# Optimization experiments

Measured on AMD Instinct MI355X. Metric: run time of the kernel, lower is better.

Reference implementation:

```python
import jax, jax.numpy as jnp
import numpy as np


def _hilbert_envelope(x1d):
    """|analytic signal| of a real 1-D signal, matching scipy.signal.hilbert."""
    N = x1d.shape[0]  # static at trace time
    h = np.zeros(N, dtype=np.float32)
    if N % 2 == 0:
        h[0] = 1.0
        h[N // 2] = 1.0
        h[1:N // 2] = 2.0
    else:
        h[0] = 1.0
        h[1:(N + 1) // 2] = 2.0
    Xf = jnp.fft.fft(x1d)
    analytic = jnp.fft.ifft(Xf * jnp.asarray(h))
    return jnp.abs(analytic)


def setup_inputs() -> dict:
    key = jax.random.key(0)
    B, L, D = 32, 4096, 64
    x = jax.random.normal(key, (B, L, D), dtype=jnp.float32)
    return {"x": x}


def reference(x):
    B, L, D = x.shape
    flat = x.reshape(-1)  # [B*L*D], one long signal as in the original
    up = jnp.clip(flat, 0.0, None)
    down = jnp.clip(-flat, 0.0, None)
    envelope_max = _hilbert_envelope(up).reshape(B, L, D)
    envelope_min = (-_hilbert_envelope(down)).reshape(B, L, D)
    avg_envelope = (envelope_max + envelope_min) * 0.5
    imf = x - avg_envelope
    # torch.std(dim=1, unbiased=True) -> ddof=1 over the time axis
    std_res = jnp.std(imf, axis=1, keepdims=True, ddof=1) + jnp.float32(0.01)
    return imf / std_res, avg_envelope
```

## Files before the change

kernel.cpp:

```cpp
#include <hip/hip_runtime.h>
#include <math.h>

#define NTOT 8388608
#define N1   2048
#define N2   4096
#define BB   32
#define LL   4096
#define DD   64

enum { M_NONE = 0, M_TW = 1, M_SCALE = 4 };

__device__ inline float2 cmul(float2 a, float2 b) {
    return make_float2(a.x*b.x - a.y*b.y, a.x*b.y + a.y*b.x);
}
__device__ inline float2 cmul_conj(float2 a, float2 b) {
    return make_float2(a.x*b.x + a.y*b.y, a.y*b.x - a.x*b.y);
}
__device__ inline float2 cadd(float2 a, float2 b){ return make_float2(a.x+b.x, a.y+b.y); }
__device__ inline float2 csub(float2 a, float2 b){ return make_float2(a.x-b.x, a.y-b.y); }
__device__ inline float2 mul_pi(float2 a){ return make_float2(-a.y, a.x); }
__device__ inline float2 mul_mi(float2 a){ return make_float2(a.y, -a.x); }
__device__ inline int pidx(int a){ return a + (a >> 4); }

template<bool INV>
__device__ inline void dft8(const float2* x, float2* y) {
    const float C = 0.70710678118654752f;
    float2 t0=cadd(x[0],x[4]), t1=cadd(x[1],x[5]), t2=cadd(x[2],x[6]), t3=cadd(x[3],x[7]);
    float2 u0=csub(x[0],x[4]), u1=csub(x[1],x[5]), u2=csub(x[2],x[6]), u3=csub(x[3],x[7]);
    if (!INV) {
        u1 = make_float2(C*(u1.x+u1.y), C*(u1.y-u1.x));
        u2 = mul_mi(u2);
        u3 = make_float2(C*(u3.y-u3.x), -C*(u3.x+u3.y));
    } else {
        u1 = make_float2(C*(u1.x-u1.y), C*(u1.y+u1.x));
        u2 = mul_pi(u2);
        u3 = make_float2(-C*(u3.x+u3.y), C*(u3.x-u3.y));
    }
    {
        float2 s0=cadd(t0,t2), s1=cadd(t1,t3), d0=csub(t0,t2);
        float2 d1 = INV ? mul_pi(csub(t1,t3)) : mul_mi(csub(t1,t3));
        y[0]=cadd(s0,s1); y[4]=csub(s0,s1); y[2]=cadd(d0,d1); y[6]=csub(d0,d1);
    }
    {
        float2 s0=cadd(u0,u2), s1=cadd(u1,u3), d0=csub(u0,u2);
        float2 d1 = INV ? mul_pi(csub(u1,u3)) : mul_mi(csub(u1,u3));
        y[1]=cadd(s0,s1); y[5]=csub(s0,s1); y[3]=cadd(d0,d1); y[7]=csub(d0,d1);
    }
}

__device__ inline void dft8_h0_inv(const float2* x, float2* y) {
    const float C = 0.70710678118654752f;
    float2 u1 = make_float2(C*(x[1].x - x[1].y), C*(x[1].y + x[1].x));
    float2 u2 = mul_pi(x[2]);
    float2 u3 = make_float2(-C*(x[3].x + x[3].y), C*(x[3].x - x[3].y));
    {
        float2 s0=cadd(x[0],x[2]), s1=cadd(x[1],x[3]), d0=csub(x[0],x[2]);
        float2 d1 = mul_pi(csub(x[1],x[3]));
        y[0]=cadd(s0,s1); y[4]=csub(s0,s1); y[2]=cadd(d0,d1); y[6]=csub(d0,d1);
    }
    {
        float2 s0=cadd(x[0],u2), s1=cadd(u1,u3), d0=csub(x[0],u2);
        float2 d1 = mul_pi(csub(u1,u3));
        y[1]=cadd(s0,s1); y[5]=csub(s0,s1); y[3]=cadd(d0,d1); y[7]=csub(d0,d1);
    }
}

template<bool INV>
__device__ inline void dft4(const float2* u, float2* y) {
    float2 s0=cadd(u[0],u[2]), s1=cadd(u[1],u[3]), d0=csub(u[0],u[2]);
    float2 d1 = INV ? mul_pi(csub(u[1],u[3])) : mul_mi(csub(u[1],u[3]));
    y[0]=cadd(s0,s1); y[2]=csub(s0,s1); y[1]=cadd(d0,d1); y[3]=csub(d0,d1);
}

template<bool INV, int SH>
__device__ inline void twiddle8(float2* y, int ps, const float2* __restrict__ T1t) {
    float2 w1 = T1t[(ps << SH) & 4095];
    float2 w2 = cmul(w1, w1);
    float2 w3 = cmul(w2, w1);
    float2 w4 = cmul(w2, w2);
    float2 w5 = cmul(w4, w1);
    float2 w6 = cmul(w3, w3);
    float2 w7 = cmul(w4, w3);
    if (!INV) {
        y[1]=cmul(y[1],w1); y[2]=cmul(y[2],w2); y[3]=cmul(y[3],w3);
        y[4]=cmul(y[4],w4); y[5]=cmul(y[5],w5); y[6]=cmul(y[6],w6); y[7]=cmul(y[7],w7);
    } else {
        y[1]=cmul_conj(y[1],w1); y[2]=cmul_conj(y[2],w2); y[3]=cmul_conj(y[3],w3);
        y[4]=cmul_conj(y[4],w4); y[5]=cmul_conj(y[5],w5); y[6]=cmul_conj(y[6],w6); y[7]=cmul_conj(y[7],w7);
    }
}

__global__ __launch_bounds__(256) void gen_tables(float2* T1, float2* T2) {
    int j = blockIdx.x * 256 + threadIdx.x;
    if (j < 4096) {
        double ang = -2.0 * M_PI * (double)j / 4096.0;
        T1[j] = make_float2((float)cos(ang), (float)sin(ang));
    } else if (j < 4096 + 2048) {
        int b = j - 4096;
        double ang = -2.0 * M_PI * (double)b / 8388608.0;
        T2[b] = make_float2((float)cos(ang), (float)sin(ang));
    }
}

__device__ inline float2 wbig(int t, const float2* __restrict__ T1t, const float2* __restrict__ T2t) {
    return cmul(T1t[t >> 11], T2t[t & 2047]);
}

template<bool INV, int MODE>
__global__ __launch_bounds__(512) void fft4096(float2* data,
                                               const float2* __restrict__ T1t,
                                               const float2* __restrict__ T2t) {
    __shared__ float2 S[4352];
    const int t = threadIdx.x;
    const int r = blockIdx.x;
    float2* base = data + (size_t)r * 4096;

    float2 x[8], y[8];
    #pragma unroll
    for (int m = 0; m < 8; ++m) x[m] = base[t + 512*m];

    #pragma unroll
    for (int st = 0; st < 3; ++st) {
        const int s = 1 << (3*st);
        const int q = t & (s - 1);
        const int ps = t - q;
        dft8<INV>(x, y);
        twiddle8<INV, 0>(y, ps, T1t);
        if (st) __syncthreads();
        #pragma unroll
        for (int k = 0; k < 8; ++k) S[pidx(8*ps + q + k*s)] = y[k];
        __syncthreads();
        #pragma unroll
        for (int m = 0; m < 8; ++m) x[m] = S[pidx(t + 512*m)];
    }
    dft8<INV>(x, y);

    if (MODE == M_TW) {
        float2 wb    = wbig(r * t, T1t, T2t);
        float2 wstep = wbig(512 * r, T1t, T2t);
        #pragma unroll
        for (int k = 0; k < 8; ++k) {
            int o = t + 512*k;
            base[o] = INV ? cmul_conj(y[k], wb) : cmul(y[k], wb);
            wb = INV ? cmul_conj(wb, wstep) : cmul(wb, wstep);
        }
    } else {
        #pragma unroll
        for (int k = 0; k < 8; ++k) {
            int o = t + 512*k;
            float2 v = y[k];
            if (MODE == M_SCALE) {
                const float sc = 1.f / 8388608.f;
                v.x *= sc; v.y *= sc;
            }
            base[o] = v;
        }
    }
}

__global__ __launch_bounds__(256) void fftmid(float2* data,
                                              const float2* __restrict__ T1t,
                                              const float2* __restrict__ T2t) {
    __shared__ float2 S[2176];
    const int t = threadIdx.x;
    const int r = blockIdx.x;
    float2* base = data + (size_t)r * 2048;

    float2 x[8], y[8];
    #pragma unroll
    for (int m = 0; m < 8; ++m) x[m] = base[t + 256*m];

    #pragma unroll
    for (int st = 0; st < 3; ++st) {
        const int s = 1 << (3*st);
        const int q = t & (s - 1);
        const int ps = t - q;
        dft8<false>(x, y);
        twiddle8<false, 1>(y, ps, T1t);
        if (st) __syncthreads();
        #pragma unroll
        for (int k = 0; k < 8; ++k) S[pidx(8*ps + q + k*s)] = y[k];
        __syncthreads();
        if (st < 2) {
            #pragma unroll
            for (int m = 0; m < 8; ++m) x[m] = S[pidx(t + 256*m)];
        }
    }
    float2 xa[4], xb[4], ya[4], yb[4];
    #pragma unroll
    for (int m = 0; m < 4; ++m) {
        xa[m] = S[pidx(t + 512*m)];
        xb[m] = S[pidx(t + 256 + 512*m)];
    }
    dft4<false>(xa, ya);
    dft4<false>(xb, yb);
    __syncthreads();
    #pragma unroll
    for (int k = 0; k < 4; ++k) {
        int o = t + 512*k;
        if (o < 1024) {
            float h = (o == 0 && r == 0) ? 1.f : 2.f;
            S[pidx(o)] = make_float2(ya[k].x * h, ya[k].y * h);
        } else if (o == 1024) {
            S[pidx(1024)] = (r == 0) ? ya[k] : make_float2(0.f, 0.f);
        }
        int o2 = o + 256;
        if (o2 < 1024) S[pidx(o2)] = make_float2(yb[k].x * 2.f, yb[k].y * 2.f);
    }
    __syncthreads();
    #pragma unroll
    for (int m = 0; m < 4; ++m) x[m] = S[pidx(t + 256*m)];
    dft8_h0_inv(x, y);
    if (t == 0) {
        float2 c = S[pidx(1024)];
        #pragma unroll
        for (int k = 0; k < 8; ++k) {
            if (k & 1) { y[k].x -= c.x; y[k].y -= c.y; }
            else       { y[k].x += c.x; y[k].y += c.y; }
        }
    }
    twiddle8<true, 1>(y, t, T1t);
    __syncthreads();
    #pragma unroll
    for (int k = 0; k < 8; ++k) S[pidx(8*t + k)] = y[k];
    __syncthreads();
    #pragma unroll
    for (int st = 1; st < 3; ++st) {
        const int s = 1 << (3*st);
        const int q = t & (s - 1);
        const int ps = t - q;
        #pragma unroll
        for (int m = 0; m < 8; ++m) x[m] = S[pidx(t + 256*m)];
        dft8<true>(x, y);
        twiddle8<true, 1>(y, ps, T1t);
        __syncthreads();
        #pragma unroll
        for (int k = 0; k < 8; ++k) S[pidx(8*ps + q + k*s)] = y[k];
        __syncthreads();
    }
    #pragma unroll
    for (int m = 0; m < 4; ++m) {
        xa[m] = S[pidx(t + 512*m)];
        xb[m] = S[pidx(t + 256 + 512*m)];
    }
    dft4<true>(xa, ya);
    dft4<true>(xb, yb);
    {
        float2 wka   = wbig(r * t, T1t, T2t);
        float2 w256  = wbig(256 * r, T1t, T2t);
        float2 w512  = cmul(w256, w256);
        float2 wkb   = cmul(wka, w256);
        #pragma unroll
        for (int k = 0; k < 4; ++k) {
            int o = t + 512*k;
            base[o]       = cmul_conj(ya[k], wka);
            base[o + 256] = cmul_conj(yb[k], wkb);
            wka = cmul(wka, w512);
            wkb = cmul(wkb, w512);
        }
    }
}

__global__ __launch_bounds__(256) void k_pre(const float* __restrict__ x, float2* __restrict__ A) {
    __shared__ float tile[32][33];
    int c0 = blockIdx.x * 32;
    int r0 = blockIdx.y * 32;
    int tx = threadIdx.x, ty = threadIdx.y;
    #pragma unroll
    for (int j = 0; j < 32; j += 8)
        tile[ty + j][tx] = x[(size_t)(r0 + ty + j) * N1 + c0 + tx];
    __syncthreads();
    #pragma unroll
    for (int j = 0; j < 32; j += 8) {
        float v = tile[tx][ty + j];
        A[(size_t)(c0 + ty + j) * N2 + r0 + tx] = make_float2(fmaxf(v, 0.f), fmaxf(-v, 0.f));
    }
}

__global__ __launch_bounds__(256) void k_trans(const float2* __restrict__ in, float2* __restrict__ out,
                                               int inCols, int inRows) {
    __shared__ float2 tile[32][33];
    int c0 = blockIdx.x * 32;
    int r0 = blockIdx.y * 32;
    int tx = threadIdx.x, ty = threadIdx.y;
    #pragma unroll
    for (int j = 0; j < 32; j += 8)
        tile[ty + j][tx] = in[(size_t)(r0 + ty + j) * inCols + c0 + tx];
    __syncthreads();
    #pragma unroll
    for (int j = 0; j < 32; j += 8)
        out[(size_t)(c0 + ty + j) * inRows + r0 + tx] = tile[tx][ty + j];
}

__global__ __launch_bounds__(256) void k_post(const float2* __restrict__ A, const float* __restrict__ x,
                                              float* __restrict__ out, float* __restrict__ part) {
    __shared__ float2 tile[32][33];
    __shared__ float red[2][8][32];
    int c0 = blockIdx.x * 32;
    int r0 = blockIdx.y * 32;
    int tx = threadIdx.x, ty = threadIdx.y;
    #pragma unroll
    for (int j = 0; j < 32; j += 8)
        tile[ty + j][tx] = A[(size_t)(r0 + ty + j) * N2 + c0 + tx];
    __syncthreads();
    float s1 = 0.f, s2 = 0.f;
    #pragma unroll
    for (int j = 0; j < 32; j += 8) {
        int n2 = c0 + ty + j;
        int n1 = r0 + tx;
        size_t n = (size_t)n2 * N1 + n1;
        float2 w = tile[tx][ty + j];
        float xv = x[n];
        float up = fmaxf(xv, 0.f);
        float dn = fmaxf(-xv, 0.f);
        float hu = w.y - dn;
        float hd = up - w.x;
        float em = sqrtf(up*up + hu*hu);
        float en = sqrtf(dn*dn + hd*hd);
        float avg = 0.5f * (em - en);
        float imf = xv - avg;
        out[NTOT + n] = avg;
        s1 += imf;
        s2 += imf * imf;
    }
    red[0][ty][tx] = s1;
    red[1][ty][tx] = s2;
    __syncthreads();
    if (ty == 0) {
        #pragma unroll
        for (int e = 1; e < 8; ++e) { s1 += red[0][e][tx]; s2 += red[1][e][tx]; }
        int slot = blockIdx.y * 128 + blockIdx.x;
        part[slot * 32 + tx]          = s1;
        part[262144 + slot * 32 + tx] = s2;
    }
}

__global__ __launch_bounds__(256) void std_final(const float* __restrict__ part, float* __restrict__ scalev) {
    int g = blockIdx.x * 256 + threadIdx.x;
    int b = g >> 6, d = g & 63;
    int dh = d >> 5, dl = d & 31;
    float s1 = 0.f, s2 = 0.f;
    for (int lq = 0; lq < 32; ++lq) {
        int by = lq * 2 + dh;
        #pragma unroll
        for (int ch = 0; ch < 4; ++ch) {
            int slot = by * 128 + b * 4 + ch;
            s1 += part[slot * 32 + dl];
            s2 += part[262144 + slot * 32 + dl];
        }
    }
    float mean = s1 / (float)LL;
    float var  = (s2 - (float)LL * mean * mean) / (float)(LL - 1);
    var = fmaxf(var, 0.f);
    scalev[g] = 1.f / (sqrtf(var) + 0.01f);
}

__global__ __launch_bounds__(256) void imf_final(const float* __restrict__ x, float* __restrict__ out,
                                                 const float* __restrict__ scalev) {
    size_t i = ((size_t)blockIdx.x * 256 + threadIdx.x) * 4;
    float4 xv = *(const float4*)(x + i);
    float4 av = *(const float4*)(out + NTOT + i);
    int b = (int)(i >> 18);
    int d = (int)(i & 63);
    const float* sc = scalev + b * 64;
    float4 v;
    v.x = (xv.x - av.x) * sc[d];
    v.y = (xv.y - av.y) * sc[d + 1];
    v.z = (xv.z - av.z) * sc[d + 2];
    v.w = (xv.w - av.w) * sc[d + 3];
    *(float4*)(out + i) = v;
}

extern "C" void kernel_launch(void* const* d_in, const int* in_sizes, int n_in,
                              void* d_out, int out_size, void* d_ws, size_t ws_size,
                              hipStream_t stream) {
    const float* x = (const float*)d_in[0];
    float* out = (float*)d_out;
    char* w = (char*)d_ws;

    float2* T1     = (float2*)w;
    float2* T2     = (float2*)(w + 32 * 1024);
    float*  scalev = (float*)(w + 48 * 1024);
    float2* A      = (float2*)(w + (1 << 20));
    float2* Bbuf   = (float2*)d_out;
    float*  part   = (float*)d_out;

    hipLaunchKernelGGL(gen_tables, dim3(24), dim3(256), 0, stream, T1, T2);

    hipLaunchKernelGGL(k_pre, dim3(N1/32, N2/32), dim3(32, 8), 0, stream, x, A);
    hipLaunchKernelGGL((fft4096<false, M_TW>), dim3(N1), dim3(512), 0, stream, A, T1, T2);
    hipLaunchKernelGGL(k_trans, dim3(N2/32, N1/32), dim3(32, 8), 0, stream, A, Bbuf, N2, N1);
    hipLaunchKernelGGL(fftmid, dim3(N2), dim3(256), 0, stream, Bbuf, T1, T2);
    hipLaunchKernelGGL(k_trans, dim3(N1/32, N2/32), dim3(32, 8), 0, stream, Bbuf, A, N1, N2);
    hipLaunchKernelGGL((fft4096<true, M_SCALE>), dim3(N1), dim3(512), 0, stream, A, T1, T2);

    hipLaunchKernelGGL(k_post, dim3(N2/32, N1/32), dim3(32, 8), 0, stream, A, x, out, part);
    hipLaunchKernelGGL(std_final, dim3(8), dim3(256), 0, stream, part, scalev);
    hipLaunchKernelGGL(imf_final, dim3(NTOT / 4 / 256), dim3(256), 0, stream, x, out, scalev);
}
```

Baseline: 203.7 us.

## Fuse twiddle table generation into k_pre and pack two rows per fftmid block

The twiddle-table generation kernel is folded into the first blocks of the pre-transpose kernel, which removes one launch. fftmid now processes two rows per 512-thread block, each half with its own shared buffer. The Hilbert mask and the start of the inverse transform are applied directly in registers, which drops a shared-memory round trip and two barriers. A possible race exists because k_pre writes the tables while fft4096 reads them later, but those are separate launches on one stream, so the ordering holds.

```diff
diff --git a/kernel.cpp b/kernel.cpp
--- a/kernel.cpp
+++ b/kernel.cpp
@@ -90,18 +90,6 @@
     }
 }
 
-__global__ __launch_bounds__(256) void gen_tables(float2* T1, float2* T2) {
-    int j = blockIdx.x * 256 + threadIdx.x;
-    if (j < 4096) {
-        double ang = -2.0 * M_PI * (double)j / 4096.0;
-        T1[j] = make_float2((float)cos(ang), (float)sin(ang));
-    } else if (j < 4096 + 2048) {
-        int b = j - 4096;
-        double ang = -2.0 * M_PI * (double)b / 8388608.0;
-        T2[b] = make_float2((float)cos(ang), (float)sin(ang));
-    }
-}
-
 __device__ inline float2 wbig(int t, const float2* __restrict__ T1t, const float2* __restrict__ T2t) {
     return cmul(T1t[t >> 11], T2t[t & 2047]);
 }
@@ -158,12 +146,14 @@
     }
 }
 
-__global__ __launch_bounds__(256) void fftmid(float2* data,
+__global__ __launch_bounds__(512) void fftmid(float2* data,
                                               const float2* __restrict__ T1t,
                                               const float2* __restrict__ T2t) {
-    __shared__ float2 S[2176];
-    const int t = threadIdx.x;
-    const int r = blockIdx.x;
+    __shared__ float2 S2[2][2176];
+    const int t    = threadIdx.x & 255;
+    const int half = threadIdx.x >> 8;
+    const int r    = (blockIdx.x << 1) | half;
+    float2* S = S2[half];
     float2* base = data + (size_t)r * 2048;
 
     float2 x[8], y[8];
@@ -194,29 +184,21 @@
     }
     dft4<false>(xa, ya);
     dft4<false>(xb, yb);
-    __syncthreads();
-    #pragma unroll
-    for (int k = 0; k < 4; ++k) {
-        int o = t + 512*k;
-        if (o < 1024) {
-            float h = (o == 0 && r == 0) ? 1.f : 2.f;
-            S[pidx(o)] = make_float2(ya[k].x * h, ya[k].y * h);
-        } else if (o == 1024) {
-            S[pidx(1024)] = (r == 0) ? ya[k] : make_float2(0.f, 0.f);
-        }
-        int o2 = o + 256;
-        if (o2 < 1024) S[pidx(o2)] = make_float2(yb[k].x * 2.f, yb[k].y * 2.f);
-    }
-    __syncthreads();
-    #pragma unroll
-    for (int m = 0; m < 4; ++m) x[m] = S[pidx(t + 256*m)];
-    dft8_h0_inv(x, y);
-    if (t == 0) {
-        float2 c = S[pidx(1024)];
-        #pragma unroll
-        for (int k = 0; k < 8; ++k) {
-            if (k & 1) { y[k].x -= c.x; y[k].y -= c.y; }
-            else       { y[k].x += c.x; y[k].y += c.y; }
+    {
+        float2 z[4];
+        float h0 = (t == 0 && r == 0) ? 1.f : 2.f;
+        z[0] = make_float2(ya[0].x * h0, ya[0].y * h0);
+        z[1] = make_float2(yb[0].x * 2.f, yb[0].y * 2.f);
+        z[2] = make_float2(ya[1].x * 2.f, ya[1].y * 2.f);
+        z[3] = make_float2(yb[1].x * 2.f, yb[1].y * 2.f);
+        dft8_h0_inv(z, y);
+        if (t == 0 && r == 0) {
+            float2 c = ya[2];
+            #pragma unroll
+            for (int k = 0; k < 8; ++k) {
+                if (k & 1) { y[k].x -= c.x; y[k].y -= c.y; }
+                else       { y[k].x += c.x; y[k].y += c.y; }
+            }
         }
     }
     twiddle8<true, 1>(y, t, T1t);
@@ -261,11 +243,23 @@
     }
 }
 
-__global__ __launch_bounds__(256) void k_pre(const float* __restrict__ x, float2* __restrict__ A) {
+__global__ __launch_bounds__(256) void k_pre(const float* __restrict__ x, float2* __restrict__ A,
+                                             float2* T1, float2* T2) {
     __shared__ float tile[32][33];
     int c0 = blockIdx.x * 32;
     int r0 = blockIdx.y * 32;
     int tx = threadIdx.x, ty = threadIdx.y;
+    if (blockIdx.y == 0 && blockIdx.x < 24) {
+        int j = blockIdx.x * 256 + ty * 32 + tx;
+        if (j < 4096) {
+            double ang = -2.0 * M_PI * (double)j / 4096.0;
+            T1[j] = make_float2((float)cos(ang), (float)sin(ang));
+        } else if (j < 4096 + 2048) {
+            int b = j - 4096;
+            double ang = -2.0 * M_PI * (double)b / 8388608.0;
+            T2[b] = make_float2((float)cos(ang), (float)sin(ang));
+        }
+    }
     #pragma unroll
     for (int j = 0; j < 32; j += 8)
         tile[ty + j][tx] = x[(size_t)(r0 + ty + j) * N1 + c0 + tx];
@@ -385,12 +379,10 @@
     float2* Bbuf   = (float2*)d_out;
     float*  part   = (float*)d_out;
 
-    hipLaunchKernelGGL(gen_tables, dim3(24), dim3(256), 0, stream, T1, T2);
-
-    hipLaunchKernelGGL(k_pre, dim3(N1/32, N2/32), dim3(32, 8), 0, stream, x, A);
+    hipLaunchKernelGGL(k_pre, dim3(N1/32, N2/32), dim3(32, 8), 0, stream, x, A, T1, T2);
     hipLaunchKernelGGL((fft4096<false, M_TW>), dim3(N1), dim3(512), 0, stream, A, T1, T2);
     hipLaunchKernelGGL(k_trans, dim3(N2/32, N1/32), dim3(32, 8), 0, stream, A, Bbuf, N2, N1);
-    hipLaunchKernelGGL(fftmid, dim3(N2), dim3(256), 0, stream, Bbuf, T1, T2);
+    hipLaunchKernelGGL(fftmid, dim3(N2/2), dim3(512), 0, stream, Bbuf, T1, T2);
     hipLaunchKernelGGL(k_trans, dim3(N1/32, N2/32), dim3(32, 8), 0, stream, Bbuf, A, N1, N2);
     hipLaunchKernelGGL((fft4096<true, M_SCALE>), dim3(N1), dim3(512), 0, stream, A, T1, T2);
 
```

After: 200.1 us. About the same (-1.8%).
